# Kernel tuning notes

Hardware: AMD Instinct MI355X
Metric: run time of the kernel (lower is better)

The kernel has to match this reference:

```python
import jax, jax.numpy as jnp
import numpy as np

B, IN_DIM, K, OUT_DIM = 512, 16384, 32, 16
DIMS = [8192, 4096, 2048]  # floor(dim/factor) per layer, factor=2


def setup_inputs() -> dict:
    key = jax.random.key(0)
    ks = jax.random.split(key, 16)
    inp = {"x": jax.random.normal(ks[0], (B, IN_DIM), dtype=jnp.float32)}
    prev = IN_DIM
    std = (2.0 / K) ** 0.5
    for i, d in enumerate(DIMS):
        inp[f"w{i}"] = jax.random.normal(ks[1 + i], (d, K), dtype=jnp.float32) * std
        inp[f"b{i}"] = jnp.zeros((1, d), dtype=jnp.float32)
        inp[f"knn{i}"] = jax.random.randint(ks[8 + i], (d, K), 0, prev, dtype=jnp.int64)
        prev = d
    inp["fc_w"] = jax.random.normal(ks[12], (DIMS[-1], OUT_DIM), dtype=jnp.float32) * (1.0 / DIMS[-1] ** 0.5)
    inp["fc_b"] = jnp.zeros((OUT_DIM,), dtype=jnp.float32)
    return inp


def reference(x, w0, b0, w1, b1, w2, b2, fc_w, fc_b, knn0, knn1, knn2):
    # Each layer: gather K neighbors per output unit, weighted sum over K, bias, ReLU.
    for w, b, knn in ((w0, b0, knn0), (w1, b1, knn1), (w2, b2, knn2)):
        g = x[:, knn]                              # (B, dim_i, K) irregular gather
        x = jax.nn.relu(jnp.einsum('bdk,dk->bd', g, w) + b)
    return x @ fc_w + fc_b                         # fc_angle
```

## Files before the change

### kernel.cpp

```cpp
#include <hip/hip_runtime.h>
#include <hip/hip_fp16.h>

#define BATCH   512
#define IN_DIM  16384
#define KNN     32

typedef __attribute__((ext_vector_type(4))) _Float16 half4v;

#define N0 (8192 * KNN)
#define N1 (4096 * KNN)
#define N2 (2048 * KNN)

__global__ __launch_bounds__(256) void prep_k(const int* __restrict__ k0,
                                              const float* __restrict__ w0,
                                              const int* __restrict__ k1,
                                              const float* __restrict__ w1,
                                              const int* __restrict__ k2,
                                              const float* __restrict__ w2,
                                              unsigned int* __restrict__ po) {
    const int t = blockIdx.x * 256 + threadIdx.x;
    int idx; float wv;
    if (t < N0) {
        idx = k0[t];            wv = w0[t];
    } else if (t < N0 + N1) {
        idx = k1[t - N0];       wv = w1[t - N0];
    } else if (t < N0 + N1 + N2) {
        idx = k2[t - N0 - N1];  wv = w2[t - N0 - N1];
    } else {
        return;
    }
    const unsigned short hb =
        __builtin_bit_cast(unsigned short, (_Float16)wv);
    po[t] = (unsigned int)(unsigned short)idx | ((unsigned int)hb << 16);
}

__global__ __launch_bounds__(256) void transpose_h(const float* __restrict__ in,
                                                   _Float16* __restrict__ out) {
    __shared__ float tile[32][33];
    const int bx = blockIdx.x * 32;
    const int by = blockIdx.y * 32;
    const int tx = threadIdx.x & 31;
    const int ty = threadIdx.x >> 5;
#pragma unroll
    for (int j = 0; j < 32; j += 8)
        tile[ty + j][tx] = in[(size_t)(by + ty + j) * IN_DIM + bx + tx];
    __syncthreads();
    const int r = threadIdx.x >> 3;
    const int c = (threadIdx.x & 7) * 4;
    half4v h;
    h[0] = (_Float16)tile[c + 0][r];
    h[1] = (_Float16)tile[c + 1][r];
    h[2] = (_Float16)tile[c + 2][r];
    h[3] = (_Float16)tile[c + 3][r];
    *(half4v*)(out + (size_t)(bx + r) * BATCH + by + c) = h;
}

__global__ __launch_bounds__(256) void lcn_p4(const _Float16* __restrict__ xt,
                                              const unsigned int* __restrict__ packed,
                                              const float* __restrict__ bias,
                                              _Float16* __restrict__ yt) {
    const int lane = threadIdx.x & 63;
    const int wv   = __builtin_amdgcn_readfirstlane(threadIdx.x >> 6);
    const int d    = (blockIdx.x >> 3) * 4 + wv;
    const int b    = (blockIdx.x & 7) * 64 + lane;
    const unsigned int* kp = packed + (size_t)d * KNN;
    const _Float16*     xb = xt + b;
    float acc = 0.f;
#pragma unroll
    for (int k = 0; k < KNN; ++k) {
        const unsigned int u = kp[k];
        const int idx = (int)(u & 0xffffu);
        const _Float16 hw =
            __builtin_bit_cast(_Float16, (unsigned short)(u >> 16));
        acc += (float)hw * (float)xb[(size_t)idx * BATCH];
    }
    acc = fmaxf(acc + bias[d], 0.f);
    yt[(size_t)d * BATCH + b] = (_Float16)acc;
}

__global__ __launch_bounds__(256) void fc_partial(const _Float16* __restrict__ y2t,
                                                  const float* __restrict__ fcw,
                                                  float* __restrict__ part) {
    const int o  = blockIdx.x & 15;
    const int bh = (blockIdx.x >> 4) & 1;
    const int ch = blockIdx.x >> 5;
    const int b  = bh * 256 + threadIdx.x;
    const int d0 = ch * 256;
    float a0 = 0.f, a1 = 0.f, a2 = 0.f, a3 = 0.f;
#pragma unroll 4
    for (int d = d0; d < d0 + 256; d += 4) {
        a0 += (float)y2t[(size_t)(d + 0) * BATCH + b] * fcw[(d + 0) * 16 + o];
        a1 += (float)y2t[(size_t)(d + 1) * BATCH + b] * fcw[(d + 1) * 16 + o];
        a2 += (float)y2t[(size_t)(d + 2) * BATCH + b] * fcw[(d + 2) * 16 + o];
        a3 += (float)y2t[(size_t)(d + 3) * BATCH + b] * fcw[(d + 3) * 16 + o];
    }
    part[((size_t)b * 16 + o) * 8 + ch] = (a0 + a1) + (a2 + a3);
}

__global__ __launch_bounds__(256) void fc_final(const float* __restrict__ part,
                                                const float* __restrict__ fcb,
                                                float* __restrict__ out) {
    const int t = blockIdx.x * 256 + threadIdx.x;
    const float4 p0 = *(const float4*)(part + (size_t)t * 8);
    const float4 p1 = *(const float4*)(part + (size_t)t * 8 + 4);
    out[t] = ((p0.x + p0.y) + (p0.z + p0.w)) + ((p1.x + p1.y) + (p1.z + p1.w))
             + fcb[t & 15];
}

extern "C" void kernel_launch(void* const* d_in, const int* in_sizes, int n_in,
                              void* d_out, int out_size, void* d_ws, size_t ws_size,
                              hipStream_t stream) {
    const float* x    = (const float*)d_in[0];
    const float* w0   = (const float*)d_in[1];
    const float* b0   = (const float*)d_in[2];
    const int*   knn0 = (const int*)  d_in[3];
    const float* w1   = (const float*)d_in[4];
    const float* b1   = (const float*)d_in[5];
    const int*   knn1 = (const int*)  d_in[6];
    const float* w2   = (const float*)d_in[7];
    const float* b2   = (const float*)d_in[8];
    const int*   knn2 = (const int*)  d_in[9];
    const float* fcw  = (const float*)d_in[10];
    const float* fcb  = (const float*)d_in[11];
    float* out = (float*)d_out;

    char* ws = (char*)d_ws;
    _Float16*     xt   = (_Float16*)(ws);
    _Float16*     y0t  = (_Float16*)(ws + ((size_t)16 << 20));
    _Float16*     y1t  = (_Float16*)(ws + ((size_t)24 << 20));
    _Float16*     y2t  = (_Float16*)(ws + ((size_t)28 << 20));
    float*        part = (float*)   (ws + ((size_t)30 << 20));
    unsigned int* po   = (unsigned int*)(ws + ((size_t)30 << 20) + ((size_t)512 << 10));

    prep_k<<<(N0 + N1 + N2 + 255) / 256, 256, 0, stream>>>(knn0, w0, knn1, w1,
                                                           knn2, w2, po);
    transpose_h<<<dim3(IN_DIM / 32, BATCH / 32), 256, 0, stream>>>(x, xt);
    lcn_p4<<<(8192 / 4) * 8, 256, 0, stream>>>(xt,  po,           b0, y0t);
    lcn_p4<<<(4096 / 4) * 8, 256, 0, stream>>>(y0t, po + N0,      b1, y1t);
    lcn_p4<<<(2048 / 4) * 8, 256, 0, stream>>>(y1t, po + N0 + N1, b2, y2t);
    fc_partial<<<256, 256, 0, stream>>>(y2t, fcw, part);
    fc_final<<<32, 256, 0, stream>>>(part, fcb, out);
}
```

Measured before the change: 70.65 us.

## Fuse prep and transpose kernels, widen layer 1-2 gathers, LDS-stage FC

Merges the weight/index packing kernel and the input transpose into one launch that splits work by block index, saving a kernel launch. Layers 1 and 2 use a new variant where each lane gathers two adjacent half-precision batch elements per neighbor index, halving the thread count and index loads. The FC partial stage now stages a 256x64 tile of the layer-2 output in shared memory, and each wave computes four output columns from it. This cuts redundant global reads of the activations, though the FC now runs only 64 blocks.

```diff
diff --git a/kernel.cpp b/kernel.cpp
--- a/kernel.cpp
+++ b/kernel.cpp
@@ -6,53 +6,55 @@
 #define KNN     32
 
 typedef __attribute__((ext_vector_type(4))) _Float16 half4v;
+typedef __attribute__((ext_vector_type(2))) _Float16 half2v;
 
 #define N0 (8192 * KNN)
 #define N1 (4096 * KNN)
 #define N2 (2048 * KNN)
+#define NPACK (N0 + N1 + N2)
+#define TR_BLOCKS (512 * 16)
+#define PREP_BLOCKS (NPACK / 256)
 
-__global__ __launch_bounds__(256) void prep_k(const int* __restrict__ k0,
-                                              const float* __restrict__ w0,
-                                              const int* __restrict__ k1,
-                                              const float* __restrict__ w1,
-                                              const int* __restrict__ k2,
-                                              const float* __restrict__ w2,
-                                              unsigned int* __restrict__ po) {
-    const int t = blockIdx.x * 256 + threadIdx.x;
-    int idx; float wv;
-    if (t < N0) {
-        idx = k0[t];            wv = w0[t];
-    } else if (t < N0 + N1) {
-        idx = k1[t - N0];       wv = w1[t - N0];
-    } else if (t < N0 + N1 + N2) {
-        idx = k2[t - N0 - N1];  wv = w2[t - N0 - N1];
+__global__ __launch_bounds__(256) void prep_tr(const float* __restrict__ in,
+                                               _Float16* __restrict__ out,
+                                               const int* __restrict__ k0,
+                                               const float* __restrict__ w0,
+                                               const int* __restrict__ k1,
+                                               const float* __restrict__ w1,
+                                               const int* __restrict__ k2,
+                                               const float* __restrict__ w2,
+                                               unsigned int* __restrict__ po) {
+    __shared__ float tile[32][33];
+    if (blockIdx.x < TR_BLOCKS) {
+        const int bx = (blockIdx.x & 511) * 32;
+        const int by = (blockIdx.x >> 9) * 32;
+        const int tx = threadIdx.x & 31;
+        const int ty = threadIdx.x >> 5;
+#pragma unroll
+        for (int j = 0; j < 32; j += 8)
+            tile[ty + j][tx] = in[(size_t)(by + ty + j) * IN_DIM + bx + tx];
+        __syncthreads();
+        const int r = threadIdx.x >> 3;
+        const int c = (threadIdx.x & 7) * 4;
+        half4v h;
+        h[0] = (_Float16)tile[c + 0][r];
+        h[1] = (_Float16)tile[c + 1][r];
+        h[2] = (_Float16)tile[c + 2][r];
+        h[3] = (_Float16)tile[c + 3][r];
+        *(half4v*)(out + (size_t)(bx + r) * BATCH + by + c) = h;
     } else {
-        return;
+        const int t = (blockIdx.x - TR_BLOCKS) * 256 + threadIdx.x;
+        int idx; float wv;
+        if (t < N0) {
+            idx = k0[t];            wv = w0[t];
+        } else if (t < N0 + N1) {
+            idx = k1[t - N0];       wv = w1[t - N0];
+        } else {
+            idx = k2[t - N0 - N1];  wv = w2[t - N0 - N1];
+        }
+        const unsigned short hb = __builtin_bit_cast(unsigned short, (_Float16)wv);
+        po[t] = (unsigned int)(unsigned short)idx | ((unsigned int)hb << 16);
     }
-    const unsigned short hb =
-        __builtin_bit_cast(unsigned short, (_Float16)wv);
-    po[t] = (unsigned int)(unsigned short)idx | ((unsigned int)hb << 16);
-}
-
-__global__ __launch_bounds__(256) void transpose_h(const float* __restrict__ in,
-                                                   _Float16* __restrict__ out) {
-    __shared__ float tile[32][33];
-    const int bx = blockIdx.x * 32;
-    const int by = blockIdx.y * 32;
-    const int tx = threadIdx.x & 31;
-    const int ty = threadIdx.x >> 5;
-#pragma unroll
-    for (int j = 0; j < 32; j += 8)
-        tile[ty + j][tx] = in[(size_t)(by + ty + j) * IN_DIM + bx + tx];
-    __syncthreads();
-    const int r = threadIdx.x >> 3;
-    const int c = (threadIdx.x & 7) * 4;
-    half4v h;
-    h[0] = (_Float16)tile[c + 0][r];
-    h[1] = (_Float16)tile[c + 1][r];
-    h[2] = (_Float16)tile[c + 2][r];
-    h[3] = (_Float16)tile[c + 3][r];
-    *(half4v*)(out + (size_t)(bx + r) * BATCH + by + c) = h;
 }
 
 __global__ __launch_bounds__(256) void lcn_p4(const _Float16* __restrict__ xt,
@@ -78,23 +80,67 @@
     yt[(size_t)d * BATCH + b] = (_Float16)acc;
 }
 
-__global__ __launch_bounds__(256) void fc_partial(const _Float16* __restrict__ y2t,
-                                                  const float* __restrict__ fcw,
-                                                  float* __restrict__ part) {
-    const int o  = blockIdx.x & 15;
-    const int bh = (blockIdx.x >> 4) & 1;
-    const int ch = blockIdx.x >> 5;
-    const int b  = bh * 256 + threadIdx.x;
-    const int d0 = ch * 256;
+__global__ __launch_bounds__(256) void lcn_p4w(const _Float16* __restrict__ xt,
+                                               const unsigned int* __restrict__ packed,
+                                               const float* __restrict__ bias,
+                                               _Float16* __restrict__ yt) {
+    const int lane = threadIdx.x & 63;
+    const int wv   = __builtin_amdgcn_readfirstlane(threadIdx.x >> 6);
+    const int d    = (blockIdx.x >> 2) * 4 + wv;
+    const int b    = (blockIdx.x & 3) * 128 + 2 * lane;
+    const unsigned int* kp = packed + (size_t)d * KNN;
+    const _Float16*     xb = xt + b;
+    float ax = 0.f, ay = 0.f;
+#pragma unroll
+    for (int k = 0; k < KNN; ++k) {
+        const unsigned int u = kp[k];
+        const int idx = (int)(u & 0xffffu);
+        const float hw =
+            (float)__builtin_bit_cast(_Float16, (unsigned short)(u >> 16));
+        const half2v v = *(const half2v*)(xb + (size_t)idx * BATCH);
+        ax += hw * (float)v[0];
+        ay += hw * (float)v[1];
+    }
+    const float bv = bias[d];
+    half2v r;
+    r[0] = (_Float16)fmaxf(ax + bv, 0.f);
+    r[1] = (_Float16)fmaxf(ay + bv, 0.f);
+    *(half2v*)(yt + (size_t)d * BATCH + b) = r;
+}
+
+__global__ __launch_bounds__(256) void fc_lds(const _Float16* __restrict__ y2t,
+                                              const float* __restrict__ fcw,
+                                              float* __restrict__ part) {
+    __shared__ _Float16 ty[256][64];
+    const int r  = blockIdx.x >> 3;
+    const int c  = blockIdx.x & 7;
+    const int rr = threadIdx.x >> 4;
+    const int c4 = (threadIdx.x & 15) * 4;
+#pragma unroll
+    for (int j = 0; j < 16; ++j) {
+        const int dl = j * 16 + rr;
+        *(half4v*)&ty[dl][c4] =
+            *(const half4v*)(y2t + (size_t)(r * 256 + dl) * BATCH + c * 64 + c4);
+    }
+    __syncthreads();
+    const int b  = threadIdx.x & 63;
+    const int wv = __builtin_amdgcn_readfirstlane(threadIdx.x >> 6);
+    const float* fw = fcw + (size_t)(r * 256) * 16 + wv * 4;
     float a0 = 0.f, a1 = 0.f, a2 = 0.f, a3 = 0.f;
 #pragma unroll 4
-    for (int d = d0; d < d0 + 256; d += 4) {
-        a0 += (float)y2t[(size_t)(d + 0) * BATCH + b] * fcw[(d + 0) * 16 + o];
-        a1 += (float)y2t[(size_t)(d + 1) * BATCH + b] * fcw[(d + 1) * 16 + o];
-        a2 += (float)y2t[(size_t)(d + 2) * BATCH + b] * fcw[(d + 2) * 16 + o];
-        a3 += (float)y2t[(size_t)(d + 3) * BATCH + b] * fcw[(d + 3) * 16 + o];
+    for (int dl = 0; dl < 256; ++dl) {
+        const float v = (float)ty[dl][b];
+        a0 += v * fw[dl * 16 + 0];
+        a1 += v * fw[dl * 16 + 1];
+        a2 += v * fw[dl * 16 + 2];
+        a3 += v * fw[dl * 16 + 3];
     }
-    part[((size_t)b * 16 + o) * 8 + ch] = (a0 + a1) + (a2 + a3);
+    const int bb = c * 64 + b;
+    float* pp = part + ((size_t)bb * 16 + wv * 4) * 8 + r;
+    pp[0]  = a0;
+    pp[8]  = a1;
+    pp[16] = a2;
+    pp[24] = a3;
 }
 
 __global__ __launch_bounds__(256) void fc_final(const float* __restrict__ part,
@@ -132,12 +178,11 @@
     float*        part = (float*)   (ws + ((size_t)30 << 20));
     unsigned int* po   = (unsigned int*)(ws + ((size_t)30 << 20) + ((size_t)512 << 10));
 
-    prep_k<<<(N0 + N1 + N2 + 255) / 256, 256, 0, stream>>>(knn0, w0, knn1, w1,
-                                                           knn2, w2, po);
-    transpose_h<<<dim3(IN_DIM / 32, BATCH / 32), 256, 0, stream>>>(x, xt);
-    lcn_p4<<<(8192 / 4) * 8, 256, 0, stream>>>(xt,  po,           b0, y0t);
-    lcn_p4<<<(4096 / 4) * 8, 256, 0, stream>>>(y0t, po + N0,      b1, y1t);
-    lcn_p4<<<(2048 / 4) * 8, 256, 0, stream>>>(y1t, po + N0 + N1, b2, y2t);
-    fc_partial<<<256, 256, 0, stream>>>(y2t, fcw, part);
+    prep_tr<<<TR_BLOCKS + PREP_BLOCKS, 256, 0, stream>>>(x, xt, knn0, w0, knn1,
+                                                         w1, knn2, w2, po);
+    lcn_p4 <<<(8192 / 4) * 8, 256, 0, stream>>>(xt,  po,           b0, y0t);
+    lcn_p4w<<<(4096 / 4) * 4, 256, 0, stream>>>(y0t, po + N0,      b1, y1t);
+    lcn_p4w<<<(2048 / 4) * 4, 256, 0, stream>>>(y1t, po + N0 + N1, b2, y2t);
+    fc_lds<<<64, 256, 0, stream>>>(y2t, fcw, part);
     fc_final<<<32, 256, 0, stream>>>(part, fcb, out);
 }
```

Result: no change. 70.88 us (+0.3%).
